# Kernel optimization log

Hardware: AMD Instinct MI355X
Metric: run time of the kernel (lower is better)

The kernel has to match this reference:

```python
import jax, jax.numpy as jnp
import numpy as np

B = 16384       # batch size
P = 2           # fixed pooling factor per bag (offsets are arange * P)
NTAB = 26       # number of sparse feature tables
NROWS = 100000  # rows per embedding table
D = 128         # embedding dim == ln_bot[-1]
LN_BOT = [13, 512, 256, 128]
LN_TOP = [479, 1024, 512, 256, 1]


def setup_inputs() -> dict:
    key = jax.random.key(0)
    ks = jax.random.split(key, 32)
    inp = {}
    inp['dense_x'] = jax.random.normal(ks[0], (B, LN_BOT[0]), dtype=jnp.float32)
    # offsets: uniform stride-P bags (EmbeddingBag offsets)
    inp['lS_o'] = jnp.broadcast_to(jnp.arange(B, dtype=jnp.int64) * P, (NTAB, B))
    inp['lS_i'] = jax.random.randint(ks[1], (NTAB, B * P), 0, NROWS, dtype=jnp.int64)
    # embedding tables, uniform(-sqrt(1/n), sqrt(1/n))
    bound = float(np.sqrt(1.0 / NROWS))
    inp['emb_tables'] = jax.random.uniform(ks[2], (NTAB, NROWS, D), dtype=jnp.float32,
                                           minval=-bound, maxval=bound)
    # bot MLP params (He-style scaled normal)
    ki = 3
    for i in range(len(LN_BOT) - 1):
        n, m = LN_BOT[i], LN_BOT[i + 1]
        inp[f'bw{i}'] = jax.random.normal(ks[ki], (m, n), dtype=jnp.float32) * np.sqrt(2.0 / (m + n)); ki += 1
        inp[f'bb{i}'] = jax.random.normal(ks[ki], (m,), dtype=jnp.float32) * np.sqrt(1.0 / m); ki += 1
    for i in range(len(LN_TOP) - 1):
        n, m = LN_TOP[i], LN_TOP[i + 1]
        inp[f'tw{i}'] = jax.random.normal(ks[ki], (m, n), dtype=jnp.float32) * np.sqrt(2.0 / (m + n)); ki += 1
        inp[f'tb{i}'] = jax.random.normal(ks[ki], (m,), dtype=jnp.float32) * np.sqrt(1.0 / m); ki += 1
    return inp


def _mlp(x, Ws, bs, sigmoid_layer):
    for i, (W, b) in enumerate(zip(Ws, bs)):
        x = x @ W.T + b
        x = jax.nn.sigmoid(x) if i == sigmoid_layer else jax.nn.relu(x)
    return x


def reference(dense_x, lS_o, lS_i, emb_tables,
              bw0, bb0, bw1, bb1, bw2, bb2,
              tw0, tb0, tw1, tb1, tw2, tb2, tw3, tb3):
    # bot MLP (sigmoid_bot = -1 -> all ReLU)
    x = _mlp(dense_x, [bw0, bw1, bw2], [bb0, bb1, bb2], sigmoid_layer=-1)  # [B, D]

    # multi-table EmbeddingBag sum pooling. Offsets (lS_o) are uniform stride-P
    # arange bags, so sum pooling is a gather + reshape + sum over P.
    def pool_one(table, idx):
        return table[idx].reshape(B, P, D).sum(axis=1)  # [B, D]
    ly = jax.vmap(pool_one)(emb_tables, lS_i)  # [NTAB, B, D]

    # dot interaction (arch_interaction_itself=False -> strict lower triangle)
    T = jnp.concatenate([x[:, None, :], jnp.transpose(ly, (1, 0, 2))], axis=1)  # [B, 27, D]
    Z = jnp.einsum('bid,bjd->bij', T, T)  # [B, 27, 27]
    ni = NTAB + 1
    li, lj = jnp.tril_indices(ni, k=-1)
    Zflat = Z[:, li, lj]  # [B, 351]
    R = jnp.concatenate([x, Zflat], axis=1)  # [B, 479]

    # top MLP (sigmoid at last layer, sigmoid_top = 3)
    p = _mlp(R, [tw0, tw1, tw2, tw3], [tb0, tb1, tb2, tb3], sigmoid_layer=3)
    return p  # [B, 1]
```

## Files before the change

kernel.cpp:

```cpp
#include <hip/hip_runtime.h>
#include <hip/hip_bf16.h>
#include <math.h>

#define BATCH 16384
#define NTAB 26
#define DIM 128
#define NROWS 100000

typedef short bf16x8 __attribute__((ext_vector_type(8)));
typedef float f32x4 __attribute__((ext_vector_type(4)));
typedef float f32x16 __attribute__((ext_vector_type(16)));

__device__ __forceinline__ ushort f2b(float f) {
  union { float f; unsigned u; } c; c.f = f;
  unsigned r = (c.u + 0x7fffu + ((c.u >> 16) & 1u)) >> 16;
  return (ushort)r;
}
__device__ __forceinline__ float b2f(ushort u) {
  union { unsigned u; float f; } c; c.u = (unsigned)u << 16;
  return c.f;
}

__device__ __forceinline__ void gload_lds16(const void* g, void* l) {
  __builtin_amdgcn_global_load_lds(
      (const __attribute__((address_space(1))) void*)g,
      (__attribute__((address_space(3))) void*)l, 16, 0, 0);
}

__global__ __launch_bounds__(256) void prep_kernel(
    const float* __restrict__ dense_x, const float* __restrict__ bw0,
    const float* __restrict__ bw1, const float* __restrict__ bw2,
    const float* __restrict__ tw0, const float* __restrict__ tw1,
    const float* __restrict__ tw2,
    ushort* __restrict__ dxp, ushort* __restrict__ wb0,
    ushort* __restrict__ o1, ushort* __restrict__ o2, ushort* __restrict__ o3,
    ushort* __restrict__ o4, ushort* __restrict__ o5) {
  int i = blockIdx.x * 256 + threadIdx.x;
  switch (blockIdx.y) {
    case 0: if (i < 256 * 512) o1[i] = f2b(bw1[i]); break;
    case 1: if (i < 128 * 256) {
      int r = i >> 8, cc = i & 255;
      int db = (((cc << 1) ^ ((r & 7) << 4)) >> 1);
      o2[r * 256 + db] = f2b(bw2[i]);
    } break;
    case 2: if (i < 1024 * 512) {
      int r = i >> 9, cc = i & 511;
      o3[i] = (cc < 479) ? f2b(tw0[(size_t)r * 479 + cc]) : (ushort)0;
    } break;
    case 3: if (i < 512 * 1024) o4[i] = f2b(tw1[i]); break;
    case 4: if (i < 256 * 512) o5[i] = f2b(tw2[i]); break;
    case 5: if (i < BATCH * 32) {
      int r = i >> 5, c = i & 31;
      dxp[i] = (c < 13) ? f2b(dense_x[r * 13 + c]) : (ushort)0;
    } break;
    case 6: if (i < 512 * 32) {
      int r = i >> 5, c = i & 31;
      wb0[i] = (c < 13) ? f2b(bw0[r * 13 + c]) : (ushort)0;
    } break;
  }
}

__global__ __launch_bounds__(256) void embint_kernel(
    const float* __restrict__ tables, const int* __restrict__ lS_i,
    const ushort* __restrict__ xb, ushort* __restrict__ R) {
  __shared__ ushort Tls[4][32 * 128];
  const int wave = threadIdx.x >> 6, lane = threadIdx.x & 63;
  const int b = blockIdx.x * 4 + wave;
  char* tl = (char*)Tls[wave];

  *(uint*)(tl + lane * 4) = *(const uint*)(xb + (size_t)b * 128 + lane * 2);
#pragma unroll
  for (int r = 27; r < 32; r++)
    *(uint*)(tl + r * 256 + ((lane * 4) ^ ((r & 7) << 4))) = 0;
#pragma unroll 8
  for (int t = 0; t < NTAB; t++) {
    const int* idx = lS_i + ((size_t)t << 15) + (b << 1);
    int i0 = idx[0], i1 = idx[1];
    float2 v0 = ((const float2*)(tables + ((size_t)t * NROWS + i0) * DIM))[lane];
    float2 v1 = ((const float2*)(tables + ((size_t)t * NROWS + i1) * DIM))[lane];
    ushort2 s; s.x = f2b(v0.x + v1.x); s.y = f2b(v0.y + v1.y);
    int row = t + 1;
    *(uint*)(tl + row * 256 + ((lane * 4) ^ ((row & 7) << 4))) = *(uint*)&s;
  }
  __syncthreads();

  const int row = lane & 31;
  const int khb = (lane >> 5) * 16;
  const int swz = (row & 7) << 4;
  f32x16 z = {};
#pragma unroll
  for (int ks = 0; ks < 8; ks++) {
    bf16x8 a = *(const bf16x8*)(tl + row * 256 + ((ks * 32 + khb) ^ swz));
    z = __builtin_amdgcn_mfma_f32_32x32x16_bf16(a, a, z, 0, 0, 0);
  }

  ushort* Rb = R + (size_t)b * 512;
  *(uint*)(Rb + lane * 2) = *(const uint*)(tl + lane * 4);
  if (lane < 33) Rb[479 + lane] = 0;
  const int j = lane & 31;
  const int rb4 = (lane >> 5) * 4;
#pragma unroll
  for (int r = 0; r < 16; r++) {
    int i = (r & 3) + 8 * (r >> 2) + rb4;
    if (i <= 26 && j < i) Rb[DIM + (i * (i - 1)) / 2 + j] = f2b(z[r]);
  }
}

#define RING_SLOT 16384
__global__ __launch_bounds__(256) void bmlp_kernel(
    const ushort* __restrict__ dxp, const ushort* __restrict__ wb0,
    const float* __restrict__ b0, const ushort* __restrict__ W1,
    const float* __restrict__ b1, const ushort* __restrict__ W2g,
    const float* __restrict__ b2, ushort* __restrict__ Y) {
  __shared__ char lds[65536 + 3 * RING_SLOT + 36864];
  char* R1 = lds;
  char* RING = lds + 65536;
  char* wb0s = lds + 65536 + 3 * RING_SLOT;
  char* dxt = wb0s + 32768;
  const int tid = threadIdx.x;
  const int lane = tid & 63, wave = tid >> 6;
  const int m0 = blockIdx.x * 64;
  const int fr = lane & 15;
  const int kqb = (lane >> 4) * 16;
  const int cl = lane & 15, rh = (lane >> 4) * 4;

  float vb0[8], vb1[4], vb2[2];
#pragma unroll
  for (int h = 0; h < 2; h++)
#pragma unroll
    for (int nf = 0; nf < 4; nf++)
      vb0[h * 4 + nf] = b0[wave * 128 + h * 64 + nf * 16 + cl];
#pragma unroll
  for (int j = 0; j < 4; j++) vb1[j] = b1[wave * 64 + j * 16 + cl];
#pragma unroll
  for (int j = 0; j < 2; j++) vb2[j] = b2[wave * 32 + j * 16 + cl];

#pragma unroll
  for (int i = 0; i < 8; i++) {
    int flat = i * 4096 + tid * 16;
    int row = flat >> 6, cb = flat & 63;
    gload_lds16(wb0 + row * 32 + (cb >> 1), wb0s + flat);
  }
  {
    int flat = tid * 16;
    int row = flat >> 6, cb = flat & 63;
    gload_lds16(dxp + (size_t)(m0 + row) * 32 + (cb >> 1), dxt + flat);
  }

  const int srow = lane >> 2;
  const int scolb = ((lane & 3) << 4) ^ ((srow & 3) << 4);
#pragma unroll
  for (int kt = 0; kt < 2; kt++)
#pragma unroll
    for (int i = 0; i < 4; i++)
      gload_lds16(W1 + (size_t)(wave * 64 + i * 16 + srow) * 512 + kt * 32 + (scolb >> 1),
                  RING + kt * RING_SLOT + wave * 4096 + i * 1024);

  asm volatile("s_waitcnt vmcnt(8)" ::: "memory");
  __builtin_amdgcn_sched_barrier(0);
  __builtin_amdgcn_s_barrier();
  __builtin_amdgcn_sched_barrier(0);

  {
    bf16x8 a0[4];
#pragma unroll
    for (int mf = 0; mf < 4; mf++)
      a0[mf] = *(const bf16x8*)(dxt + (mf * 16 + fr) * 64 + kqb);
#pragma unroll
    for (int h = 0; h < 2; h++) {
      f32x4 acc0[4][4] = {};
#pragma unroll
      for (int nf = 0; nf < 4; nf++) {
        int wrow = wave * 128 + h * 64 + nf * 16 + fr;
        bf16x8 bb = *(const bf16x8*)(wb0s + wrow * 64 + kqb);
#pragma unroll
        for (int mf = 0; mf < 4; mf++)
          acc0[mf][nf] = __builtin_amdgcn_mfma_f32_16x16x32_bf16(a0[mf], bb, acc0[mf][nf], 0, 0, 0);
      }
#pragma unroll
      for (int nf = 0; nf < 4; nf++) {
        int n = wave * 128 + h * 64 + nf * 16 + cl;
#pragma unroll
        for (int mf = 0; mf < 4; mf++)
#pragma unroll
          for (int r = 0; r < 4; r++) {
            int row = mf * 16 + rh + r;
            float v = fmaxf(acc0[mf][nf][r] + vb0[h * 4 + nf], 0.f);
            *(ushort*)(R1 + row * 1024 + ((2 * n) ^ ((row & 7) << 4))) = f2b(v);
          }
      }
    }
  }
  asm volatile("s_waitcnt lgkmcnt(0)" ::: "memory");
  __builtin_amdgcn_sched_barrier(0);
  __builtin_amdgcn_s_barrier();
  __builtin_amdgcn_sched_barrier(0);

  f32x4 acc1[4][4] = {};
  const int fswz = (fr & 3) << 4;
  for (int kt = 0; kt < 16; kt++) {
    if (kt < 15) { asm volatile("s_waitcnt vmcnt(4)" ::: "memory"); }
    else         { asm volatile("s_waitcnt vmcnt(0)" ::: "memory"); }
    __builtin_amdgcn_sched_barrier(0);
    __builtin_amdgcn_s_barrier();
    __builtin_amdgcn_sched_barrier(0);

    const char* W1s = RING + (kt % 3) * RING_SLOT;
    bf16x8 a[4], w[4];
#pragma unroll
    for (int i = 0; i < 4; i++) {
      int row = i * 16 + fr;
      a[i] = *(const bf16x8*)(R1 + row * 1024 + ((kt * 64 + kqb) ^ ((row & 7) << 4)));
    }
#pragma unroll
    for (int j = 0; j < 4; j++)
      w[j] = *(const bf16x8*)(W1s + (wave * 64 + j * 16 + fr) * 64 + (kqb ^ fswz));

    if (kt + 2 < 16) {
#pragma unroll
      for (int i = 0; i < 4; i++)
        gload_lds16(W1 + (size_t)(wave * 64 + i * 16 + srow) * 512 + (kt + 2) * 32 + (scolb >> 1),
                    RING + ((kt + 2) % 3) * RING_SLOT + wave * 4096 + i * 1024);
    }

    asm volatile("s_waitcnt lgkmcnt(0)" ::: "memory");
    __builtin_amdgcn_sched_barrier(0);
    __builtin_amdgcn_s_setprio(1);
#pragma unroll
    for (int i = 0; i < 4; i++)
#pragma unroll
      for (int j = 0; j < 4; j++)
        acc1[i][j] = __builtin_amdgcn_mfma_f32_16x16x32_bf16(a[i], w[j], acc1[i][j], 0, 0, 0);
    __builtin_amdgcn_s_setprio(0);
  }

  __builtin_amdgcn_s_barrier();

#pragma unroll
  for (int i = 0; i < 16; i++)
    gload_lds16(W2g + i * 2048 + tid * 8, R1 + i * 4096 + tid * 16);

  char* C1 = RING;
#pragma unroll
  for (int j = 0; j < 4; j++) {
    int n = wave * 64 + j * 16 + cl;
#pragma unroll
    for (int i = 0; i < 4; i++) {
      int rw = i * 16 + rh;
#pragma unroll
      for (int r = 0; r < 4; r++)
        *(ushort*)(C1 + (size_t)(rw + r) * 520 + n * 2) = f2b(fmaxf(acc1[i][j][r] + vb1[j], 0.f));
    }
  }
  __syncthreads();

  f32x4 acc2[4][2] = {};
#pragma unroll
  for (int ks = 0; ks < 8; ks++) {
    const int kb = ks * 64 + kqb;
    bf16x8 a2[4], w2[2];
#pragma unroll
    for (int i = 0; i < 4; i++)
      a2[i] = *(const bf16x8*)(C1 + (i * 16 + fr) * 520 + kb);
#pragma unroll
    for (int j = 0; j < 2; j++)
      w2[j] = *(const bf16x8*)(R1 + (wave * 32 + j * 16 + fr) * 512 + (kb ^ ((fr & 7) << 4)));
#pragma unroll
    for (int i = 0; i < 4; i++)
#pragma unroll
      for (int j = 0; j < 2; j++)
        acc2[i][j] = __builtin_amdgcn_mfma_f32_16x16x32_bf16(a2[i], w2[j], acc2[i][j], 0, 0, 0);
  }
#pragma unroll
  for (int j = 0; j < 2; j++) {
    int n = wave * 32 + j * 16 + cl;
#pragma unroll
    for (int i = 0; i < 4; i++) {
      int mb = m0 + i * 16 + rh;
#pragma unroll
      for (int r = 0; r < 4; r++)
        Y[(size_t)(mb + r) * 128 + n] = f2b(fmaxf(acc2[i][j][r] + vb2[j], 0.f));
    }
  }
}

#define SLOT_BYTES 49152
template <int ACT>
__global__ __launch_bounds__(512, 2) void gemm256_kernel(
    const ushort* __restrict__ A, const ushort* __restrict__ W,
    const float* __restrict__ bias, ushort* __restrict__ C, int K, int ldc) {
  __shared__ char lds[3 * SLOT_BYTES];
  const int tid = threadIdx.x;
  const int lane = tid & 63, wid = tid >> 6;
  const int wm = wid >> 2, wn = wid & 3;

  const int nwg = gridDim.x * gridDim.y;
  const int orig = blockIdx.y * gridDim.x + blockIdx.x;
  const int q = nwg >> 3, r8 = nwg & 7;
  const int xcd = orig & 7, pos = orig >> 3;
  const int swzid = (xcd < r8 ? xcd * (q + 1) : r8 * (q + 1) + (xcd - r8) * q) + pos;
  const int m0 = (swzid / gridDim.x) * 256, n0 = (swzid % gridDim.x) * 128;
  const int NK = K >> 6;

  const int srow = tid >> 3;
  const int scolb = (tid & 7) << 4;

#pragma unroll
  for (int kt = 0; kt < 2; kt++) {
    char* As = lds + kt * SLOT_BYTES;
    char* Bs = As + 32768;
    const int k0 = kt * 64;
#pragma unroll
    for (int i = 0; i < 4; i++) {
      int row = i * 64 + srow;
      int colb = scolb ^ ((row & 7) << 4);
      gload_lds16(A + (size_t)(m0 + row) * K + k0 + (colb >> 1), As + i * 8192 + wid * 1024);
    }
#pragma unroll
    for (int i = 0; i < 2; i++) {
      int row = i * 64 + srow;
      int colb = scolb ^ ((row & 7) << 4);
      gload_lds16(W + (size_t)(n0 + row) * K + k0 + (colb >> 1), Bs + i * 8192 + wid * 1024);
    }
  }

  f32x4 acc[8][2] = {};
  const int fr = lane & 15;
  const int fkb = (lane >> 4) * 16;

  for (int kt = 0; kt < NK; kt++) {
    if (kt + 1 < NK) { asm volatile("s_waitcnt vmcnt(6)" ::: "memory"); }
    else             { asm volatile("s_waitcnt vmcnt(0)" ::: "memory"); }
    __builtin_amdgcn_sched_barrier(0);
    __builtin_amdgcn_s_barrier();
    __builtin_amdgcn_sched_barrier(0);

    const char* As = lds + (kt % 3) * SLOT_BYTES;
    const char* Bs = As + 32768;
    char* Ad = lds + ((kt + 2) % 3) * SLOT_BYTES;
    char* Bd = Ad + 32768;
    const int k2 = (kt + 2) * 64;
    const bool do_stage = (kt + 2 < NK);

#pragma unroll
    for (int kh = 0; kh < 2; kh++) {
      bf16x8 a[8], b[2];
#pragma unroll
      for (int mf = 0; mf < 8; mf++) {
        int row = wm * 128 + mf * 16 + fr;
        int colb = (kh * 64 + fkb) ^ ((row & 7) << 4);
        a[mf] = *(const bf16x8*)(As + row * 128 + colb);
      }
#pragma unroll
      for (int nf = 0; nf < 2; nf++) {
        int row = wn * 32 + nf * 16 + fr;
        int colb = (kh * 64 + fkb) ^ ((row & 7) << 4);
        b[nf] = *(const bf16x8*)(Bs + row * 128 + colb);
      }
      if (do_stage) {
#pragma unroll
        for (int i = kh * 2; i < kh * 2 + 2; i++) {
          int row = i * 64 + srow;
          int colb = scolb ^ ((row & 7) << 4);
          gload_lds16(A + (size_t)(m0 + row) * K + k2 + (colb >> 1), Ad + i * 8192 + wid * 1024);
        }
        {
          int row = kh * 64 + srow;
          int colb = scolb ^ ((row & 7) << 4);
          gload_lds16(W + (size_t)(n0 + row) * K + k2 + (colb >> 1), Bd + kh * 8192 + wid * 1024);
        }
      }
      __builtin_amdgcn_sched_barrier(0);
      __builtin_amdgcn_s_barrier();
      asm volatile("s_waitcnt lgkmcnt(0)" ::: "memory");
      __builtin_amdgcn_sched_barrier(0);
      __builtin_amdgcn_s_setprio(1);
#pragma unroll
      for (int mf = 0; mf < 8; mf++)
#pragma unroll
        for (int nf = 0; nf < 2; nf++)
          acc[mf][nf] = __builtin_amdgcn_mfma_f32_16x16x32_bf16(a[mf], b[nf], acc[mf][nf], 0, 0, 0);
      __builtin_amdgcn_s_setprio(0);
      if (kh == 0) {
        __builtin_amdgcn_sched_barrier(0);
        __builtin_amdgcn_s_barrier();
        __builtin_amdgcn_sched_barrier(0);
      }
    }
  }

  const int cr = lane & 15, rh = (lane >> 4) * 4;
#pragma unroll
  for (int nf = 0; nf < 2; nf++) {
    int n = n0 + wn * 32 + nf * 16 + cr;
    float bs = bias[n];
#pragma unroll
    for (int mf = 0; mf < 8; mf++) {
      int mb = m0 + wm * 128 + mf * 16 + rh;
#pragma unroll
      for (int r = 0; r < 4; r++) {
        float v = acc[mf][nf][r] + bs;
        if (ACT) v = fmaxf(v, 0.f);
        C[(size_t)(mb + r) * ldc + n] = f2b(v);
      }
    }
  }
}

__global__ __launch_bounds__(256) void t2final_kernel(
    const ushort* __restrict__ A, const ushort* __restrict__ W,
    const float* __restrict__ bias, const float* __restrict__ w3,
    const float* __restrict__ b3, float* __restrict__ out) {
  __shared__ char smem[64 * 264 * 2];
  ushort* As = (ushort*)smem;
  ushort* Bs = (ushort*)(smem + 4096);
  ushort* Ct = (ushort*)smem;
  const int tid = threadIdx.x;
  const int lane = tid & 63, wave = tid >> 6;
  const int m0 = blockIdx.x * 64;

  const int srow = lane >> 2;
  const int scolb = ((lane & 3) << 4) ^ ((srow & 3) << 4);
  const ushort* Ag = A + (size_t)(m0 + wave * 16 + srow) * 512 + (scolb >> 1);
  const ushort* Wg = W + (size_t)(wave * 16 + srow) * 512 + (scolb >> 1);

  f32x4 acc[4][4] = {};
  const int fr = lane & 15;
  const int fkb = (lane >> 4) * 16;
  const int fswz = (fr & 3) << 4;

  for (int k0 = 0; k0 < 512; k0 += 32) {
    gload_lds16(Ag + k0, (char*)As + wave * 1024);
#pragma unroll
    for (int i = 0; i < 4; i++)
      gload_lds16(Wg + (size_t)(i * 64) * 512 + k0, (char*)Bs + i * 4096 + wave * 1024);
    __syncthreads();
    bf16x8 a[4], b[4];
#pragma unroll
    for (int i = 0; i < 4; i++) {
      a[i] = *(const bf16x8*)((const char*)As + (i * 16 + fr) * 64 + (fkb ^ fswz));
      b[i] = *(const bf16x8*)((const char*)Bs + (wave * 64 + i * 16 + fr) * 64 + (fkb ^ fswz));
    }
#pragma unroll
    for (int i = 0; i < 4; i++)
#pragma unroll
      for (int j = 0; j < 4; j++)
        acc[i][j] = __builtin_amdgcn_mfma_f32_16x16x32_bf16(a[i], b[j], acc[i][j], 0, 0, 0);
    __syncthreads();
  }

  const int col_l = lane & 15, row_h = (lane >> 4) * 4;
#pragma unroll
  for (int j = 0; j < 4; j++) {
    int n = wave * 64 + j * 16 + col_l;
    float bs = bias[n];
#pragma unroll
    for (int i = 0; i < 4; i++) {
      int mb = i * 16 + row_h;
#pragma unroll
      for (int r = 0; r < 4; r++)
        Ct[(size_t)(mb + r) * 264 + n] = f2b(fmaxf(acc[i][j][r] + bs, 0.f));
    }
  }
  __syncthreads();

  const float4 wv = ((const float4*)w3)[lane];
  const float bf = b3[0];
  for (int rr = 0; rr < 16; rr++) {
    int row = wave * 16 + rr;
    ushort4 a4 = *(const ushort4*)&Ct[(size_t)row * 264 + lane * 4];
    float s = b2f(a4.x) * wv.x + b2f(a4.y) * wv.y + b2f(a4.z) * wv.z + b2f(a4.w) * wv.w;
#pragma unroll
    for (int off = 32; off >= 1; off >>= 1) s += __shfl_xor(s, off);
    if (lane == 0) out[m0 + row] = 1.f / (1.f + expf(-(s + bf)));
  }
}

extern "C" void kernel_launch(void* const* d_in, const int* in_sizes, int n_in,
                              void* d_out, int out_size, void* d_ws, size_t ws_size,
                              hipStream_t stream) {
  const float* dense_x = (const float*)d_in[0];
  const int* lS_i = (const int*)d_in[2];
  const float* emb = (const float*)d_in[3];
  const float* bw0 = (const float*)d_in[4];
  const float* bb0 = (const float*)d_in[5];
  const float* bw1 = (const float*)d_in[6];
  const float* bb1 = (const float*)d_in[7];
  const float* bw2 = (const float*)d_in[8];
  const float* bb2 = (const float*)d_in[9];
  const float* tw0 = (const float*)d_in[10];
  const float* tb0 = (const float*)d_in[11];
  const float* tw1 = (const float*)d_in[12];
  const float* tb1 = (const float*)d_in[13];
  const float* tw2 = (const float*)d_in[14];
  const float* tb2 = (const float*)d_in[15];
  const float* tw3 = (const float*)d_in[16];
  const float* tb3 = (const float*)d_in[17];
  float* out = (float*)d_out;

  char* w = (char*)d_ws;
  ushort* xb  = (ushort*)w; w += (size_t)BATCH * 128 * 2;
  ushort* x1  = (ushort*)w; w += (size_t)BATCH * 512 * 2;
  ushort* x2  = (ushort*)w; w += (size_t)BATCH * 256 * 2;
  ushort* R   = (ushort*)w; w += (size_t)BATCH * 512 * 2;
  ushort* t1  = (ushort*)w; w += (size_t)BATCH * 1024 * 2;
  ushort* wb1 = (ushort*)w; w += 256 * 512 * 2;
  ushort* wb2 = (ushort*)w; w += 128 * 256 * 2;
  ushort* wt0 = (ushort*)w; w += 1024 * 512 * 2;
  ushort* wt1 = (ushort*)w; w += 512 * 1024 * 2;
  ushort* wt2 = (ushort*)w; w += 256 * 512 * 2;
  ushort* dxp = (ushort*)w; w += (size_t)BATCH * 32 * 2;
  ushort* wb0 = (ushort*)w; w += 512 * 32 * 2;
  ushort* t2 = x1;
  (void)x2;

  prep_kernel<<<dim3(2048, 7), 256, 0, stream>>>(
      dense_x, bw0, bw1, bw2, tw0, tw1, tw2, dxp, wb0,
      wb1, wb2, wt0, wt1, wt2);

  bmlp_kernel<<<BATCH / 64, 256, 0, stream>>>(dxp, wb0, bb0, wb1, bb1, wb2, bb2, xb);

  embint_kernel<<<BATCH / 4, 256, 0, stream>>>(emb, lS_i, xb, R);

  gemm256_kernel<1><<<dim3(1024 / 128, BATCH / 256), 512, 0, stream>>>(R,  wt0, tb0, t1, 512, 1024);
  gemm256_kernel<1><<<dim3(512 / 128,  BATCH / 256), 512, 0, stream>>>(t1, wt1, tb1, t2, 1024, 512);
  t2final_kernel<<<BATCH / 64, 256, 0, stream>>>(t2, wt2, tb2, tw3, tb3, out);
}
```

Measured before the change: 186.6 us.

## Shrink GEMM K-tile to 32 and raise occupancy to four blocks per CU

After: 186.1 us. About the same (-0.3%).

```diff
diff --git a/kernel.cpp b/kernel.cpp
--- a/kernel.cpp
+++ b/kernel.cpp
@@ -284,9 +284,9 @@
   }
 }
 
-#define SLOT_BYTES 49152
+#define SLOT_BYTES 24576
 template <int ACT>
-__global__ __launch_bounds__(512, 2) void gemm256_kernel(
+__global__ __launch_bounds__(512, 4) void gemm256_kernel(
     const ushort* __restrict__ A, const ushort* __restrict__ W,
     const float* __restrict__ bias, ushort* __restrict__ C, int K, int ldc) {
   __shared__ char lds[3 * SLOT_BYTES];
@@ -300,93 +300,79 @@
   const int xcd = orig & 7, pos = orig >> 3;
   const int swzid = (xcd < r8 ? xcd * (q + 1) : r8 * (q + 1) + (xcd - r8) * q) + pos;
   const int m0 = (swzid / gridDim.x) * 256, n0 = (swzid % gridDim.x) * 128;
-  const int NK = K >> 6;
-
-  const int srow = tid >> 3;
-  const int scolb = (tid & 7) << 4;
+  const int NK = K >> 5;
+
+  const int arow0 = tid >> 2;
+  const int acb = (tid & 3) << 4;
+
+  f32x4 acc[8][2] = {};
+  const int fr = lane & 15;
+  const int kqb = (lane >> 4) * 16;
 
 #pragma unroll
   for (int kt = 0; kt < 2; kt++) {
     char* As = lds + kt * SLOT_BYTES;
-    char* Bs = As + 32768;
-    const int k0 = kt * 64;
-#pragma unroll
-    for (int i = 0; i < 4; i++) {
-      int row = i * 64 + srow;
-      int colb = scolb ^ ((row & 7) << 4);
-      gload_lds16(A + (size_t)(m0 + row) * K + k0 + (colb >> 1), As + i * 8192 + wid * 1024);
-    }
+    char* Bs = As + 16384;
+    const int k0 = kt * 32;
 #pragma unroll
     for (int i = 0; i < 2; i++) {
-      int row = i * 64 + srow;
-      int colb = scolb ^ ((row & 7) << 4);
-      gload_lds16(W + (size_t)(n0 + row) * K + k0 + (colb >> 1), Bs + i * 8192 + wid * 1024);
-    }
-  }
-
-  f32x4 acc[8][2] = {};
-  const int fr = lane & 15;
-  const int fkb = (lane >> 4) * 16;
+      int row = i * 128 + arow0;
+      int cb = acb ^ ((row & 3) << 4);
+      gload_lds16(A + (size_t)(m0 + row) * K + k0 + (cb >> 1), As + i * 8192 + tid * 16);
+    }
+    {
+      int cb = acb ^ ((arow0 & 3) << 4);
+      gload_lds16(W + (size_t)(n0 + arow0) * K + k0 + (cb >> 1), Bs + tid * 16);
+    }
+  }
 
   for (int kt = 0; kt < NK; kt++) {
-    if (kt + 1 < NK) { asm volatile("s_waitcnt vmcnt(6)" ::: "memory"); }
+    if (kt + 1 < NK) { asm volatile("s_waitcnt vmcnt(3)" ::: "memory"); }
     else             { asm volatile("s_waitcnt vmcnt(0)" ::: "memory"); }
     __builtin_amdgcn_sched_barrier(0);
     __builtin_amdgcn_s_barrier();
     __builtin_amdgcn_sched_barrier(0);
 
     const char* As = lds + (kt % 3) * SLOT_BYTES;
-    const char* Bs = As + 32768;
-    char* Ad = lds + ((kt + 2) % 3) * SLOT_BYTES;
-    char* Bd = Ad + 32768;
-    const int k2 = (kt + 2) * 64;
-    const bool do_stage = (kt + 2 < NK);
-
-#pragma unroll
-    for (int kh = 0; kh < 2; kh++) {
-      bf16x8 a[8], b[2];
-#pragma unroll
-      for (int mf = 0; mf < 8; mf++) {
-        int row = wm * 128 + mf * 16 + fr;
-        int colb = (kh * 64 + fkb) ^ ((row & 7) << 4);
-        a[mf] = *(const bf16x8*)(As + row * 128 + colb);
+    const char* Bs = As + 16384;
+
+    bf16x8 a[8], b[2];
+#pragma unroll
+    for (int mf = 0; mf < 8; mf++) {
+      int row = wm * 128 + mf * 16 + fr;
+      a[mf] = *(const bf16x8*)(As + row * 64 + (kqb ^ ((row & 3) << 4)));
+    }
+#pragma unroll
+    for (int nf = 0; nf < 2; nf++) {
+      int row = wn * 32 + nf * 16 + fr;
+      b[nf] = *(const bf16x8*)(Bs + row * 64 + (kqb ^ ((row & 3) << 4)));
+    }
+
+    if (kt + 2 < NK) {
+      char* Ad = lds + ((kt + 2) % 3) * SLOT_BYTES;
+      char* Bd = Ad + 16384;
+      const int k2 = (kt + 2) * 32;
+#pragma unroll
+      for (int i = 0; i < 2; i++) {
+        int row = i * 128 + arow0;
+        int cb = acb ^ ((row & 3) << 4);
+        gload_lds16(A + (size_t)(m0 + row) * K + k2 + (cb >> 1), Ad + i * 8192 + tid * 16);
       }
-#pragma unroll
-      for (int nf = 0; nf < 2; nf++) {
-        int row = wn * 32 + nf * 16 + fr;
-        int colb = (kh * 64 + fkb) ^ ((row & 7) << 4);
-        b[nf] = *(const bf16x8*)(Bs + row * 128 + colb);
+      {
+        int cb = acb ^ ((arow0 & 3) << 4);
+        gload_lds16(W + (size_t)(n0 + arow0) * K + k2 + (cb >> 1), Bd + tid * 16);
       }
-      if (do_stage) {
-#pragma unroll
-        for (int i = kh * 2; i < kh * 2 + 2; i++) {
-          int row = i * 64 + srow;
-          int colb = scolb ^ ((row & 7) << 4);
-          gload_lds16(A + (size_t)(m0 + row) * K + k2 + (colb >> 1), Ad + i * 8192 + wid * 1024);
-        }
-        {
-          int row = kh * 64 + srow;
-          int colb = scolb ^ ((row & 7) << 4);
-          gload_lds16(W + (size_t)(n0 + row) * K + k2 + (colb >> 1), Bd + kh * 8192 + wid * 1024);
-        }
-      }
-      __builtin_amdgcn_sched_barrier(0);
-      __builtin_amdgcn_s_barrier();
-      asm volatile("s_waitcnt lgkmcnt(0)" ::: "memory");
-      __builtin_amdgcn_sched_barrier(0);
-      __builtin_amdgcn_s_setprio(1);
-#pragma unroll
-      for (int mf = 0; mf < 8; mf++)
-#pragma unroll
-        for (int nf = 0; nf < 2; nf++)
-          acc[mf][nf] = __builtin_amdgcn_mfma_f32_16x16x32_bf16(a[mf], b[nf], acc[mf][nf], 0, 0, 0);
-      __builtin_amdgcn_s_setprio(0);
-      if (kh == 0) {
-        __builtin_amdgcn_sched_barrier(0);
-        __builtin_amdgcn_s_barrier();
-        __builtin_amdgcn_sched_barrier(0);
-      }
-    }
+    }
+
+    asm volatile("s_waitcnt lgkmcnt(0)" ::: "memory");
+    __builtin_amdgcn_sched_barrier(0);
+    __builtin_amdgcn_s_setprio(1);
+#pragma unroll
+    for (int mf = 0; mf < 8; mf++)
+#pragma unroll
+      for (int nf = 0; nf < 2; nf++)
+        acc[mf][nf] = __builtin_amdgcn_mfma_f32_16x16x32_bf16(a[mf], b[nf], acc[mf][nf], 0, 0, 0);
+    __builtin_amdgcn_s_setprio(0);
   }
 
   const int cr = lane & 15, rh = (lane >> 4) * 4;
```
